# Performance work log

Hardware: AMD Instinct MI355X
Metric: run time of the kernel (lower is better)

## Reference

```python
import jax, jax.numpy as jnp
import numpy as np

N_NODES = 50000
LEAK = 0.01  # torch F.leaky_relu default negative_slope


def _gcn_conv(xg, ei, W, b):
    # Standard GCNConv: add self-loops, symmetric deg^-1/2 normalization, scatter-add.
    # xg: [N, 10], ei: [2, E] int
    n = xg.shape[0]
    loop = jnp.arange(n, dtype=ei.dtype)
    src = jnp.concatenate([ei[0], loop])  # [E+N]
    dst = jnp.concatenate([ei[1], loop])
    deg = jax.ops.segment_sum(jnp.ones_like(dst, dtype=xg.dtype), dst, num_segments=n)
    dinv = jnp.where(deg > 0, jax.lax.rsqrt(jnp.maximum(deg, 1.0)), 0.0)
    h = xg @ W  # [N, 10]
    norm = (dinv[src] * dinv[dst])[:, None]  # [E+N, 1]
    out = jax.ops.segment_sum(h[src] * norm, dst, num_segments=n)  # [N, 10]
    return out + b


def setup_inputs() -> dict:
    key = jax.random.key(0)
    ks = jax.random.split(key, 12)
    B, N, E = 32, N_NODES, 800000
    in_dim, out_dim = 20, 4
    x = jax.random.normal(ks[0], (B, in_dim // 2), dtype=jnp.float32)
    gcn_x = jax.random.normal(ks[1], (B, N, 10), dtype=jnp.float32)
    gcn_edge_index = jax.random.randint(ks[2], (B, 2, E), 0, N, dtype=jnp.int64 if jax.config.jax_enable_x64 else jnp.int32)
    s = lambda fan_in: 1.0 / np.sqrt(fan_in)
    W_gcn = jax.random.uniform(ks[3], (10, 10), jnp.float32, -s(10), s(10))
    b_gcn = jax.random.uniform(ks[4], (10,), jnp.float32, -s(10), s(10))
    W1 = jax.random.uniform(ks[5], (in_dim, 4 * in_dim), jnp.float32, -s(in_dim), s(in_dim))
    b1 = jax.random.uniform(ks[6], (4 * in_dim,), jnp.float32, -s(in_dim), s(in_dim))
    W2 = jax.random.uniform(ks[7], (4 * in_dim, 8 * in_dim), jnp.float32, -s(4 * in_dim), s(4 * in_dim))
    b2 = jax.random.uniform(ks[8], (8 * in_dim,), jnp.float32, -s(4 * in_dim), s(4 * in_dim))
    Wo = jax.random.uniform(ks[9], (8 * in_dim, out_dim), jnp.float32, -s(8 * in_dim), s(8 * in_dim))
    bo = jax.random.uniform(ks[10], (out_dim,), jnp.float32, -s(8 * in_dim), s(8 * in_dim))
    return {"x": x, "gcn_x": gcn_x, "gcn_edge_index": gcn_edge_index,
            "W_gcn": W_gcn, "b_gcn": b_gcn, "W1": W1, "b1": b1,
            "W2": W2, "b2": b2, "Wo": Wo, "bo": bo}


def reference(x, gcn_x, gcn_edge_index, W_gcn, b_gcn, W1, b1, W2, b2, Wo, bo):
    # batched GCN over independent graphs (vectorized version of the per-sample loop)
    gcn_out = jax.vmap(lambda xg, ei: _gcn_conv(xg, ei, W_gcn, b_gcn))(gcn_x, gcn_edge_index)
    pooled = jnp.mean(gcn_out, axis=1)  # [B, 10]
    h = jnp.concatenate([pooled, x], axis=1)  # [B, 20]
    h = jax.nn.leaky_relu(h @ W1 + b1, negative_slope=LEAK)
    h = jax.nn.leaky_relu(h @ W2 + b2, negative_slope=LEAK)
    h = jax.nn.log_softmax(h @ Wo + bo, axis=0)  # F.log_softmax(..., 0)
    return jnp.squeeze(h, axis=0) if h.shape[0] == 1 else h  # out_dim != 1 -> squeeze(0)
```

## Files before the change

kernel.cpp:

```cpp
#include <hip/hip_runtime.h>

#define N_NODES 50000
#define N_EDGES 800000
#define BATCH   32
#define NWORD8  12500
#define NWORDC  25000
#define CHUNKS  8
#define EPC4    25000
#define HCHUNKS 16
#define HEPC4   12500
#define QSCALE  255.0f
#define PTHREADS 640

__global__ __launch_bounds__(1024) void hist_kernel(const int* __restrict__ ei,
                                                    unsigned* __restrict__ partials) {
    const int chunk = blockIdx.x, b = blockIdx.y;
    __shared__ unsigned cnt[NWORD8];
    for (int i = threadIdx.x; i < NWORD8; i += 1024) cnt[i] = 0;
    __syncthreads();
    const int4* __restrict__ dst4 =
        (const int4*)(ei + (size_t)b * (2 * N_EDGES) + N_EDGES) + (size_t)chunk * HEPC4;
    for (int i = threadIdx.x; i < HEPC4; i += 1024) {
        const int4 v = dst4[i];
        atomicAdd(&cnt[((unsigned)v.x) >> 2], 1u << ((v.x & 3) * 8));
        atomicAdd(&cnt[((unsigned)v.y) >> 2], 1u << ((v.y & 3) * 8));
        atomicAdd(&cnt[((unsigned)v.z) >> 2], 1u << ((v.z & 3) * 8));
        atomicAdd(&cnt[((unsigned)v.w) >> 2], 1u << ((v.w & 3) * 8));
    }
    __syncthreads();
    unsigned* __restrict__ out = partials + (size_t)(b * HCHUNKS + chunk) * NWORD8;
    for (int i = threadIdx.x; i < NWORD8; i += 1024) out[i] = cnt[i];
}

__global__ void dinv_kernel(const unsigned* __restrict__ partials,
                            float* __restrict__ dinv,
                            unsigned* __restrict__ qd8) {
    const int idx = blockIdx.x * 256 + threadIdx.x;
    if (idx >= BATCH * NWORD8) return;
    const int b = idx / NWORD8, i = idx - b * NWORD8;
    const unsigned* __restrict__ p = partials + (size_t)(b * HCHUNKS) * NWORD8 + i;
    unsigned d0 = 0, d1 = 0, d2 = 0, d3 = 0;
#pragma unroll
    for (int c = 0; c < HCHUNKS; ++c) {
        const unsigned v = p[(size_t)c * NWORD8];
        d0 += v & 0xFF; d1 += (v >> 8) & 0xFF; d2 += (v >> 16) & 0xFF; d3 += v >> 24;
    }
    const float i0 = rsqrtf((float)(d0 + 1));
    const float i1 = rsqrtf((float)(d1 + 1));
    const float i2 = rsqrtf((float)(d2 + 1));
    const float i3 = rsqrtf((float)(d3 + 1));
    float4* dv4 = (float4*)(dinv + (size_t)b * N_NODES) + i;
    *dv4 = make_float4(i0, i1, i2, i3);
    const unsigned q0 = __float2uint_rn(i0 * QSCALE);
    const unsigned q1 = __float2uint_rn(i1 * QSCALE);
    const unsigned q2 = __float2uint_rn(i2 * QSCALE);
    const unsigned q3 = __float2uint_rn(i3 * QSCALE);
    qd8[(size_t)b * NWORD8 + i] = q0 | (q1 << 8) | (q2 << 16) | (q3 << 24);
}

__global__ __launch_bounds__(1024) void cscat_kernel(const int* __restrict__ ei,
                                                     const unsigned* __restrict__ qd8,
                                                     unsigned* __restrict__ cpart) {
    extern __shared__ unsigned smem[];
    unsigned* cs = smem;
    const unsigned char* qs = (const unsigned char*)(smem + NWORDC);
    const int id = blockIdx.x;
    const int b = (id & 7) + 8 * ((id >> 3) & 3);
    const int chunk = id >> 5;
    for (int i = threadIdx.x; i < NWORDC; i += 1024) cs[i] = 0;
    {
        const unsigned* __restrict__ src = qd8 + (size_t)b * NWORD8;
        unsigned* dst = smem + NWORDC;
        for (int i = threadIdx.x; i < NWORD8; i += 1024) dst[i] = src[i];
    }
    __syncthreads();
    const int* eb = ei + (size_t)b * (2 * N_EDGES);
    const int4* __restrict__ src4 = (const int4*)eb + (size_t)chunk * EPC4;
    const int4* __restrict__ dst4 = (const int4*)(eb + N_EDGES) + (size_t)chunk * EPC4;
    for (int i = threadIdx.x; i < EPC4; i += 1024) {
        const int4 s4 = src4[i];
        const int4 d4 = dst4[i];
        const unsigned q0 = qs[d4.x];
        const unsigned q1 = qs[d4.y];
        const unsigned q2 = qs[d4.z];
        const unsigned q3 = qs[d4.w];
        atomicAdd(&cs[((unsigned)s4.x) >> 1], q0 << ((s4.x & 1) << 4));
        atomicAdd(&cs[((unsigned)s4.y) >> 1], q1 << ((s4.y & 1) << 4));
        atomicAdd(&cs[((unsigned)s4.z) >> 1], q2 << ((s4.z & 1) << 4));
        atomicAdd(&cs[((unsigned)s4.w) >> 1], q3 << ((s4.w & 1) << 4));
    }
    __syncthreads();
    unsigned* __restrict__ out = cpart + (size_t)(b * CHUNKS + chunk) * NWORDC;
    for (int i = threadIdx.x; i < NWORDC; i += 1024) out[i] = cs[i];
}

__global__ void w_kernel(const unsigned* __restrict__ cpart,
                         const float* __restrict__ dinv,
                         float* __restrict__ w) {
    const int idx = blockIdx.x * 256 + threadIdx.x;
    if (idx >= BATCH * NWORDC) return;
    const int b = idx / NWORDC, i = idx - b * NWORDC;
    const unsigned* __restrict__ p = cpart + (size_t)(b * CHUNKS) * NWORDC + i;
    unsigned c0 = 0, c1 = 0;
#pragma unroll
    for (int c = 0; c < CHUNKS; ++c) {
        const unsigned v = p[(size_t)c * NWORDC];
        c0 += v & 0xFFFF; c1 += v >> 16;
    }
    const int node = 2 * i;
    const float2 d = *((const float2*)(dinv + (size_t)b * N_NODES + node));
    const float f0 = (float)c0 * (1.0f / QSCALE);
    const float f1 = (float)c1 * (1.0f / QSCALE);
    *((float2*)(w + (size_t)b * N_NODES + node)) = make_float2(d.x * (f0 + d.x), d.y * (f1 + d.y));
}

__global__ __launch_bounds__(PTHREADS) void pool_kernel(const float* __restrict__ xg,
                                                        const float* __restrict__ w,
                                                        float* __restrict__ spart) {
    const int chunk = blockIdx.x, b = blockIdx.y;
    const float4* __restrict__ xg4 = (const float4*)xg;
    const int base4 = b * 125000 + chunk * 15625;
    const int r = (4 * threadIdx.x) % 10;
    float a0 = 0.0f, a1 = 0.0f, a2 = 0.0f, a3 = 0.0f;
    for (int j = threadIdx.x; j < 15625; j += PTHREADS) {
        const int f4 = base4 + j;
        const int e0 = f4 * 4;
        const float4 v = xg4[f4];
        const float w0 = w[e0 / 10];
        const float w1 = (r == 8) ? w[e0 / 10 + 1] : w0;
        a0 += v.x * w0;
        a1 += v.y * w0;
        a2 += v.z * w1;
        a3 += v.w * w1;
    }
    __shared__ float sacc[PTHREADS / 64][10];
    const int wave = threadIdx.x >> 6;
    if ((threadIdx.x & 63) < 10) sacc[wave][threadIdx.x & 63] = 0.0f;
    __syncthreads();
    atomicAdd(&sacc[wave][r], a0);
    atomicAdd(&sacc[wave][(r + 1) % 10], a1);
    atomicAdd(&sacc[wave][(r + 2) % 10], a2);
    atomicAdd(&sacc[wave][(r + 3) % 10], a3);
    __syncthreads();
    if (threadIdx.x < 10) {
        float v = 0.0f;
#pragma unroll
        for (int wv = 0; wv < PTHREADS / 64; ++wv) v += sacc[wv][threadIdx.x];
        spart[(b * CHUNKS + chunk) * 16 + threadIdx.x] = v;
    }
}

__global__ __launch_bounds__(512) void mlp_kernel(const float* __restrict__ spart,
                           const float* __restrict__ x,
                           const float* __restrict__ W_gcn,
                           const float* __restrict__ b_gcn,
                           const float* __restrict__ W1, const float* __restrict__ b1,
                           const float* __restrict__ W2, const float* __restrict__ b2,
                           const float* __restrict__ Wo, const float* __restrict__ bo,
                           float* __restrict__ out) {
    __shared__ float ssum[32][10];
    __shared__ float h0[32][20];
    __shared__ float h1[32][80];
    __shared__ float h2[32][160];
    __shared__ float o[32][4];
    const int tid = threadIdx.x;

    for (int idx = tid; idx < 32 * 10; idx += blockDim.x) {
        const int b = idx / 10, k = idx % 10;
        float v = 0.0f;
#pragma unroll
        for (int c = 0; c < CHUNKS; ++c) v += spart[(b * CHUNKS + c) * 16 + k];
        ssum[b][k] = v;
    }
    __syncthreads();

    for (int idx = tid; idx < 32 * 20; idx += blockDim.x) {
        const int b = idx / 20, j = idx % 20;
        float v;
        if (j < 10) {
            v = 0.0f;
#pragma unroll
            for (int k = 0; k < 10; ++k) v += ssum[b][k] * W_gcn[k * 10 + j];
            v = v * (1.0f / (float)N_NODES) + b_gcn[j];
        } else {
            v = x[b * 10 + (j - 10)];
        }
        h0[b][j] = v;
    }
    __syncthreads();

    for (int idx = tid; idx < 32 * 80; idx += blockDim.x) {
        const int b = idx / 80, j = idx % 80;
        float v = b1[j];
#pragma unroll
        for (int k = 0; k < 20; ++k) v += h0[b][k] * W1[k * 80 + j];
        h1[b][j] = (v > 0.0f) ? v : 0.01f * v;
    }
    __syncthreads();

    for (int idx = tid; idx < 32 * 160; idx += blockDim.x) {
        const int b = idx / 160, j = idx % 160;
        float v = b2[j];
        for (int k = 0; k < 80; ++k) v += h1[b][k] * W2[k * 160 + j];
        h2[b][j] = (v > 0.0f) ? v : 0.01f * v;
    }
    __syncthreads();

    for (int idx = tid; idx < 32 * 4; idx += blockDim.x) {
        const int b = idx / 4, j = idx % 4;
        float v = bo[j];
        for (int k = 0; k < 160; ++k) v += h2[b][k] * Wo[k * 4 + j];
        o[b][j] = v;
    }
    __syncthreads();

    if (tid < 4) {
        float m = -1e30f;
        for (int b = 0; b < 32; ++b) m = fmaxf(m, o[b][tid]);
        float lse = 0.0f;
        for (int b = 0; b < 32; ++b) lse += expf(o[b][tid] - m);
        lse = logf(lse);
        for (int b = 0; b < 32; ++b) out[b * 4 + tid] = o[b][tid] - m - lse;
    }
}

extern "C" void kernel_launch(void* const* d_in, const int* in_sizes, int n_in,
                              void* d_out, int out_size, void* d_ws, size_t ws_size,
                              hipStream_t stream) {
    const float* x      = (const float*)d_in[0];
    const float* gcn_x  = (const float*)d_in[1];
    const int*   ei     = (const int*)d_in[2];
    const float* W_gcn  = (const float*)d_in[3];
    const float* b_gcn  = (const float*)d_in[4];
    const float* W1     = (const float*)d_in[5];
    const float* b1     = (const float*)d_in[6];
    const float* W2     = (const float*)d_in[7];
    const float* b2     = (const float*)d_in[8];
    const float* Wo     = (const float*)d_in[9];
    const float* bo     = (const float*)d_in[10];
    float* out = (float*)d_out;

    unsigned* partials = (unsigned*)d_ws;
    float*    dinv     = (float*)((char*)d_ws + (size_t)512 * NWORD8 * 4);
    unsigned* qd8      = (unsigned*)((char*)dinv + (size_t)BATCH * N_NODES * 4);
    float*    w        = (float*)((char*)qd8 + (size_t)BATCH * NWORD8 * 4);
    float*    spart    = (float*)((char*)w + (size_t)BATCH * N_NODES * 4);

    hipFuncSetAttribute((const void*)cscat_kernel,
                        hipFuncAttributeMaxDynamicSharedMemorySize,
                        (NWORDC + NWORD8) * 4);

    {
        dim3 grid(HCHUNKS, BATCH);
        hist_kernel<<<grid, 1024, 0, stream>>>(ei, partials);
    }
    {
        const int n = BATCH * NWORD8;
        dinv_kernel<<<(n + 255) / 256, 256, 0, stream>>>(partials, dinv, qd8);
    }
    {
        cscat_kernel<<<256, 1024, (NWORDC + NWORD8) * 4, stream>>>(ei, qd8, partials);
    }
    {
        const int n = BATCH * NWORDC;
        w_kernel<<<(n + 255) / 256, 256, 0, stream>>>(partials, dinv, w);
    }
    {
        dim3 grid(CHUNKS, BATCH);
        pool_kernel<<<grid, PTHREADS, 0, stream>>>(gcn_x, w, spart);
    }
    mlp_kernel<<<1, 512, 0, stream>>>(spart, x, W_gcn, b_gcn, W1, b1, W2, b2, Wo, bo, out);
}
```

Baseline: 409.3 us.

## Fuse all GCN stages into one cooperative persistent kernel with grid syncs

Replaces six separate launches with a single cooperative kernel of 256 blocks that runs the histogram, normalization, scatter, pooling and MLP phases, separated by grid.sync. The per-node weights are now computed into LDS inside the pooling phase rather than written to global memory and read back, and the histogram is split into 8 chunks instead of 16. This removes launch gaps and a global round trip for w, at the cost of grid-wide barriers, a single block running the MLP tail, and a requirement that all 256 blocks be co-resident.

```diff
diff --git a/kernel.cpp b/kernel.cpp
--- a/kernel.cpp
+++ b/kernel.cpp
@@ -1,4 +1,7 @@
 #include <hip/hip_runtime.h>
+#include <hip/hip_cooperative_groups.h>
+
+namespace cg = cooperative_groups;
 
 #define N_NODES 50000
 #define N_EDGES 800000
@@ -7,226 +10,228 @@
 #define NWORDC  25000
 #define CHUNKS  8
 #define EPC4    25000
-#define HCHUNKS 16
-#define HEPC4   12500
 #define QSCALE  255.0f
-#define PTHREADS 640
-
-__global__ __launch_bounds__(1024) void hist_kernel(const int* __restrict__ ei,
-                                                    unsigned* __restrict__ partials) {
-    const int chunk = blockIdx.x, b = blockIdx.y;
-    __shared__ unsigned cnt[NWORD8];
-    for (int i = threadIdx.x; i < NWORD8; i += 1024) cnt[i] = 0;
-    __syncthreads();
-    const int4* __restrict__ dst4 =
-        (const int4*)(ei + (size_t)b * (2 * N_EDGES) + N_EDGES) + (size_t)chunk * HEPC4;
-    for (int i = threadIdx.x; i < HEPC4; i += 1024) {
-        const int4 v = dst4[i];
-        atomicAdd(&cnt[((unsigned)v.x) >> 2], 1u << ((v.x & 3) * 8));
-        atomicAdd(&cnt[((unsigned)v.y) >> 2], 1u << ((v.y & 3) * 8));
-        atomicAdd(&cnt[((unsigned)v.z) >> 2], 1u << ((v.z & 3) * 8));
-        atomicAdd(&cnt[((unsigned)v.w) >> 2], 1u << ((v.w & 3) * 8));
-    }
-    __syncthreads();
-    unsigned* __restrict__ out = partials + (size_t)(b * HCHUNKS + chunk) * NWORD8;
-    for (int i = threadIdx.x; i < NWORD8; i += 1024) out[i] = cnt[i];
-}
-
-__global__ void dinv_kernel(const unsigned* __restrict__ partials,
-                            float* __restrict__ dinv,
-                            unsigned* __restrict__ qd8) {
-    const int idx = blockIdx.x * 256 + threadIdx.x;
-    if (idx >= BATCH * NWORD8) return;
-    const int b = idx / NWORD8, i = idx - b * NWORD8;
-    const unsigned* __restrict__ p = partials + (size_t)(b * HCHUNKS) * NWORD8 + i;
-    unsigned d0 = 0, d1 = 0, d2 = 0, d3 = 0;
-#pragma unroll
-    for (int c = 0; c < HCHUNKS; ++c) {
-        const unsigned v = p[(size_t)c * NWORD8];
-        d0 += v & 0xFF; d1 += (v >> 8) & 0xFF; d2 += (v >> 16) & 0xFF; d3 += v >> 24;
-    }
-    const float i0 = rsqrtf((float)(d0 + 1));
-    const float i1 = rsqrtf((float)(d1 + 1));
-    const float i2 = rsqrtf((float)(d2 + 1));
-    const float i3 = rsqrtf((float)(d3 + 1));
-    float4* dv4 = (float4*)(dinv + (size_t)b * N_NODES) + i;
-    *dv4 = make_float4(i0, i1, i2, i3);
-    const unsigned q0 = __float2uint_rn(i0 * QSCALE);
-    const unsigned q1 = __float2uint_rn(i1 * QSCALE);
-    const unsigned q2 = __float2uint_rn(i2 * QSCALE);
-    const unsigned q3 = __float2uint_rn(i3 * QSCALE);
-    qd8[(size_t)b * NWORD8 + i] = q0 | (q1 << 8) | (q2 << 16) | (q3 << 24);
-}
-
-__global__ __launch_bounds__(1024) void cscat_kernel(const int* __restrict__ ei,
-                                                     const unsigned* __restrict__ qd8,
-                                                     unsigned* __restrict__ cpart) {
+#define ACTIVE  1020
+#define DYNLDS  ((NWORDC + NWORD8) * 4)
+
+__global__ __launch_bounds__(1024, 1) void mega_kernel(
+    const int* __restrict__ ei, const float* __restrict__ xg,
+    const float* __restrict__ x,
+    const float* __restrict__ W_gcn, const float* __restrict__ b_gcn,
+    const float* __restrict__ W1, const float* __restrict__ b1,
+    const float* __restrict__ W2, const float* __restrict__ b2,
+    const float* __restrict__ Wo, const float* __restrict__ bo,
+    unsigned* __restrict__ partials,
+    float* __restrict__ dinv,
+    unsigned* __restrict__ qd8,
+    float* __restrict__ spart,
+    float* __restrict__ out)
+{
     extern __shared__ unsigned smem[];
-    unsigned* cs = smem;
-    const unsigned char* qs = (const unsigned char*)(smem + NWORDC);
-    const int id = blockIdx.x;
-    const int b = (id & 7) + 8 * ((id >> 3) & 3);
-    const int chunk = id >> 5;
-    for (int i = threadIdx.x; i < NWORDC; i += 1024) cs[i] = 0;
+    cg::grid_group grid = cg::this_grid();
+    const int bid = blockIdx.x;
+    const int tid = threadIdx.x;
+
     {
-        const unsigned* __restrict__ src = qd8 + (size_t)b * NWORD8;
-        unsigned* dst = smem + NWORDC;
-        for (int i = threadIdx.x; i < NWORD8; i += 1024) dst[i] = src[i];
-    }
-    __syncthreads();
-    const int* eb = ei + (size_t)b * (2 * N_EDGES);
-    const int4* __restrict__ src4 = (const int4*)eb + (size_t)chunk * EPC4;
-    const int4* __restrict__ dst4 = (const int4*)(eb + N_EDGES) + (size_t)chunk * EPC4;
-    for (int i = threadIdx.x; i < EPC4; i += 1024) {
-        const int4 s4 = src4[i];
-        const int4 d4 = dst4[i];
-        const unsigned q0 = qs[d4.x];
-        const unsigned q1 = qs[d4.y];
-        const unsigned q2 = qs[d4.z];
-        const unsigned q3 = qs[d4.w];
-        atomicAdd(&cs[((unsigned)s4.x) >> 1], q0 << ((s4.x & 1) << 4));
-        atomicAdd(&cs[((unsigned)s4.y) >> 1], q1 << ((s4.y & 1) << 4));
-        atomicAdd(&cs[((unsigned)s4.z) >> 1], q2 << ((s4.z & 1) << 4));
-        atomicAdd(&cs[((unsigned)s4.w) >> 1], q3 << ((s4.w & 1) << 4));
-    }
-    __syncthreads();
-    unsigned* __restrict__ out = cpart + (size_t)(b * CHUNKS + chunk) * NWORDC;
-    for (int i = threadIdx.x; i < NWORDC; i += 1024) out[i] = cs[i];
-}
-
-__global__ void w_kernel(const unsigned* __restrict__ cpart,
-                         const float* __restrict__ dinv,
-                         float* __restrict__ w) {
-    const int idx = blockIdx.x * 256 + threadIdx.x;
-    if (idx >= BATCH * NWORDC) return;
-    const int b = idx / NWORDC, i = idx - b * NWORDC;
-    const unsigned* __restrict__ p = cpart + (size_t)(b * CHUNKS) * NWORDC + i;
-    unsigned c0 = 0, c1 = 0;
-#pragma unroll
-    for (int c = 0; c < CHUNKS; ++c) {
-        const unsigned v = p[(size_t)c * NWORDC];
-        c0 += v & 0xFFFF; c1 += v >> 16;
-    }
-    const int node = 2 * i;
-    const float2 d = *((const float2*)(dinv + (size_t)b * N_NODES + node));
-    const float f0 = (float)c0 * (1.0f / QSCALE);
-    const float f1 = (float)c1 * (1.0f / QSCALE);
-    *((float2*)(w + (size_t)b * N_NODES + node)) = make_float2(d.x * (f0 + d.x), d.y * (f1 + d.y));
-}
-
-__global__ __launch_bounds__(PTHREADS) void pool_kernel(const float* __restrict__ xg,
-                                                        const float* __restrict__ w,
-                                                        float* __restrict__ spart) {
-    const int chunk = blockIdx.x, b = blockIdx.y;
-    const float4* __restrict__ xg4 = (const float4*)xg;
-    const int base4 = b * 125000 + chunk * 15625;
-    const int r = (4 * threadIdx.x) % 10;
-    float a0 = 0.0f, a1 = 0.0f, a2 = 0.0f, a3 = 0.0f;
-    for (int j = threadIdx.x; j < 15625; j += PTHREADS) {
-        const int f4 = base4 + j;
-        const int e0 = f4 * 4;
-        const float4 v = xg4[f4];
-        const float w0 = w[e0 / 10];
-        const float w1 = (r == 8) ? w[e0 / 10 + 1] : w0;
-        a0 += v.x * w0;
-        a1 += v.y * w0;
-        a2 += v.z * w1;
-        a3 += v.w * w1;
-    }
-    __shared__ float sacc[PTHREADS / 64][10];
-    const int wave = threadIdx.x >> 6;
-    if ((threadIdx.x & 63) < 10) sacc[wave][threadIdx.x & 63] = 0.0f;
-    __syncthreads();
-    atomicAdd(&sacc[wave][r], a0);
-    atomicAdd(&sacc[wave][(r + 1) % 10], a1);
-    atomicAdd(&sacc[wave][(r + 2) % 10], a2);
-    atomicAdd(&sacc[wave][(r + 3) % 10], a3);
-    __syncthreads();
-    if (threadIdx.x < 10) {
-        float v = 0.0f;
-#pragma unroll
-        for (int wv = 0; wv < PTHREADS / 64; ++wv) v += sacc[wv][threadIdx.x];
-        spart[(b * CHUNKS + chunk) * 16 + threadIdx.x] = v;
-    }
-}
-
-__global__ __launch_bounds__(512) void mlp_kernel(const float* __restrict__ spart,
-                           const float* __restrict__ x,
-                           const float* __restrict__ W_gcn,
-                           const float* __restrict__ b_gcn,
-                           const float* __restrict__ W1, const float* __restrict__ b1,
-                           const float* __restrict__ W2, const float* __restrict__ b2,
-                           const float* __restrict__ Wo, const float* __restrict__ bo,
-                           float* __restrict__ out) {
-    __shared__ float ssum[32][10];
-    __shared__ float h0[32][20];
-    __shared__ float h1[32][80];
-    __shared__ float h2[32][160];
-    __shared__ float o[32][4];
-    const int tid = threadIdx.x;
-
-    for (int idx = tid; idx < 32 * 10; idx += blockDim.x) {
-        const int b = idx / 10, k = idx % 10;
-        float v = 0.0f;
-#pragma unroll
-        for (int c = 0; c < CHUNKS; ++c) v += spart[(b * CHUNKS + c) * 16 + k];
-        ssum[b][k] = v;
-    }
-    __syncthreads();
-
-    for (int idx = tid; idx < 32 * 20; idx += blockDim.x) {
-        const int b = idx / 20, j = idx % 20;
-        float v;
-        if (j < 10) {
-            v = 0.0f;
-#pragma unroll
-            for (int k = 0; k < 10; ++k) v += ssum[b][k] * W_gcn[k * 10 + j];
-            v = v * (1.0f / (float)N_NODES) + b_gcn[j];
-        } else {
-            v = x[b * 10 + (j - 10)];
-        }
-        h0[b][j] = v;
-    }
-    __syncthreads();
-
-    for (int idx = tid; idx < 32 * 80; idx += blockDim.x) {
-        const int b = idx / 80, j = idx % 80;
-        float v = b1[j];
-#pragma unroll
-        for (int k = 0; k < 20; ++k) v += h0[b][k] * W1[k * 80 + j];
-        h1[b][j] = (v > 0.0f) ? v : 0.01f * v;
-    }
-    __syncthreads();
-
-    for (int idx = tid; idx < 32 * 160; idx += blockDim.x) {
-        const int b = idx / 160, j = idx % 160;
-        float v = b2[j];
-        for (int k = 0; k < 80; ++k) v += h1[b][k] * W2[k * 160 + j];
-        h2[b][j] = (v > 0.0f) ? v : 0.01f * v;
-    }
-    __syncthreads();
-
-    for (int idx = tid; idx < 32 * 4; idx += blockDim.x) {
-        const int b = idx / 4, j = idx % 4;
-        float v = bo[j];
-        for (int k = 0; k < 160; ++k) v += h2[b][k] * Wo[k * 4 + j];
-        o[b][j] = v;
-    }
-    __syncthreads();
-
-    if (tid < 4) {
-        float m = -1e30f;
-        for (int b = 0; b < 32; ++b) m = fmaxf(m, o[b][tid]);
-        float lse = 0.0f;
-        for (int b = 0; b < 32; ++b) lse += expf(o[b][tid] - m);
-        lse = logf(lse);
-        for (int b = 0; b < 32; ++b) out[b * 4 + tid] = o[b][tid] - m - lse;
+        unsigned* cnt = smem;
+        for (int i = tid; i < NWORD8; i += 1024) cnt[i] = 0;
+        __syncthreads();
+        const int b = bid >> 3, oct = bid & 7;
+        const int4* __restrict__ dst4 =
+            (const int4*)(ei + (size_t)b * (2 * N_EDGES) + N_EDGES) + (size_t)oct * EPC4;
+        for (int i = tid; i < EPC4; i += 1024) {
+            const int4 v = dst4[i];
+            atomicAdd(&cnt[((unsigned)v.x) >> 2], 1u << ((v.x & 3) * 8));
+            atomicAdd(&cnt[((unsigned)v.y) >> 2], 1u << ((v.y & 3) * 8));
+            atomicAdd(&cnt[((unsigned)v.z) >> 2], 1u << ((v.z & 3) * 8));
+            atomicAdd(&cnt[((unsigned)v.w) >> 2], 1u << ((v.w & 3) * 8));
+        }
+        __syncthreads();
+        unsigned* __restrict__ o8 = partials + (size_t)bid * NWORD8;
+        for (int i = tid; i < NWORD8; i += 1024) o8[i] = cnt[i];
+    }
+    __threadfence();
+    grid.sync();
+
+    for (int idx = bid * 1024 + tid; idx < BATCH * NWORD8; idx += 256 * 1024) {
+        const int b = idx / NWORD8, i = idx - b * NWORD8;
+        const unsigned* __restrict__ p = partials + (size_t)(b * CHUNKS) * NWORD8 + i;
+        unsigned d0 = 0, d1 = 0, d2 = 0, d3 = 0;
+#pragma unroll
+        for (int c = 0; c < CHUNKS; ++c) {
+            const unsigned v = p[(size_t)c * NWORD8];
+            d0 += v & 0xFF; d1 += (v >> 8) & 0xFF; d2 += (v >> 16) & 0xFF; d3 += v >> 24;
+        }
+        const float i0 = rsqrtf((float)(d0 + 1));
+        const float i1 = rsqrtf((float)(d1 + 1));
+        const float i2 = rsqrtf((float)(d2 + 1));
+        const float i3 = rsqrtf((float)(d3 + 1));
+        float4* dv4 = (float4*)(dinv + (size_t)b * N_NODES) + i;
+        *dv4 = make_float4(i0, i1, i2, i3);
+        const unsigned q0 = __float2uint_rn(i0 * QSCALE);
+        const unsigned q1 = __float2uint_rn(i1 * QSCALE);
+        const unsigned q2 = __float2uint_rn(i2 * QSCALE);
+        const unsigned q3 = __float2uint_rn(i3 * QSCALE);
+        qd8[(size_t)b * NWORD8 + i] = q0 | (q1 << 8) | (q2 << 16) | (q3 << 24);
+    }
+    __threadfence();
+    grid.sync();
+
+    {
+        unsigned* cs = smem;
+        const unsigned char* qs = (const unsigned char*)(smem + NWORDC);
+        const int b = bid & 31, chunk = bid >> 5;
+        for (int i = tid; i < NWORDC; i += 1024) cs[i] = 0;
+        const unsigned* __restrict__ qsrc = qd8 + (size_t)b * NWORD8;
+        for (int i = tid; i < NWORD8; i += 1024) smem[NWORDC + i] = qsrc[i];
+        __syncthreads();
+        const int* eb = ei + (size_t)b * (2 * N_EDGES);
+        const int4* __restrict__ s4p = (const int4*)eb + (size_t)chunk * EPC4;
+        const int4* __restrict__ d4p = (const int4*)(eb + N_EDGES) + (size_t)chunk * EPC4;
+        for (int i = tid; i < EPC4; i += 1024) {
+            const int4 s4 = s4p[i];
+            const int4 d4 = d4p[i];
+            const unsigned q0 = qs[d4.x];
+            const unsigned q1 = qs[d4.y];
+            const unsigned q2 = qs[d4.z];
+            const unsigned q3 = qs[d4.w];
+            atomicAdd(&cs[((unsigned)s4.x) >> 1], q0 << ((s4.x & 1) << 4));
+            atomicAdd(&cs[((unsigned)s4.y) >> 1], q1 << ((s4.y & 1) << 4));
+            atomicAdd(&cs[((unsigned)s4.z) >> 1], q2 << ((s4.z & 1) << 4));
+            atomicAdd(&cs[((unsigned)s4.w) >> 1], q3 << ((s4.w & 1) << 4));
+        }
+        __syncthreads();
+        unsigned* __restrict__ op = partials + (size_t)(b * CHUNKS + chunk) * NWORDC;
+        for (int i = tid; i < NWORDC; i += 1024) op[i] = cs[i];
+    }
+    __threadfence();
+    grid.sync();
+
+    {
+        float* wlds = (float*)smem;
+        float* sacc = (float*)smem + 6256;
+        const int c = bid & 7, b = bid >> 3;
+        const int wbase = c * (NWORDC / 8);
+        for (int i = tid; i < NWORDC / 8; i += 1024) {
+            const unsigned* __restrict__ p =
+                partials + (size_t)(b * CHUNKS) * NWORDC + wbase + i;
+            unsigned c0 = 0, c1 = 0;
+#pragma unroll
+            for (int ch = 0; ch < CHUNKS; ++ch) {
+                const unsigned v = p[(size_t)ch * NWORDC];
+                c0 += v & 0xFFFF; c1 += v >> 16;
+            }
+            const int node = 2 * (wbase + i);
+            const float2 d = *((const float2*)(dinv + (size_t)b * N_NODES + node));
+            wlds[2 * i]     = d.x * ((float)c0 * (1.0f / QSCALE) + d.x);
+            wlds[2 * i + 1] = d.y * ((float)c1 * (1.0f / QSCALE) + d.y);
+        }
+        const int wave = tid >> 6;
+        if ((tid & 63) < 10) sacc[wave * 10 + (tid & 63)] = 0.0f;
+        __syncthreads();
+        if (tid < ACTIVE) {
+            const float4* __restrict__ xg4 = (const float4*)xg;
+            const int base4 = b * 125000 + c * 15625;
+            const int r = (4 * tid) % 10;
+            float a0 = 0.0f, a1 = 0.0f, a2 = 0.0f, a3 = 0.0f;
+            for (int j = tid; j < 15625; j += ACTIVE) {
+                const float4 v = xg4[base4 + j];
+                const int ln = (4 * j) / 10;
+                const float w0 = wlds[ln];
+                const float w1 = (r == 8) ? wlds[ln + 1] : w0;
+                a0 += v.x * w0;
+                a1 += v.y * w0;
+                a2 += v.z * w1;
+                a3 += v.w * w1;
+            }
+            atomicAdd(&sacc[wave * 10 + r], a0);
+            atomicAdd(&sacc[wave * 10 + (r + 1) % 10], a1);
+            atomicAdd(&sacc[wave * 10 + (r + 2) % 10], a2);
+            atomicAdd(&sacc[wave * 10 + (r + 3) % 10], a3);
+        }
+        __syncthreads();
+        if (tid < 10) {
+            float v = 0.0f;
+#pragma unroll
+            for (int wv = 0; wv < 16; ++wv) v += sacc[wv * 10 + tid];
+            spart[(b * CHUNKS + c) * 16 + tid] = v;
+        }
+    }
+    __threadfence();
+    grid.sync();
+
+    if (bid == 0) {
+        float* fs   = (float*)smem;
+        float* ssum = fs;
+        float* h0   = fs + 320;
+        float* h1   = fs + 960;
+        float* h2   = fs + 3520;
+        float* o    = fs + 8640;
+
+        for (int idx = tid; idx < 32 * 10; idx += 1024) {
+            const int b = idx / 10, k = idx % 10;
+            float v = 0.0f;
+#pragma unroll
+            for (int c = 0; c < CHUNKS; ++c) v += spart[(b * CHUNKS + c) * 16 + k];
+            ssum[b * 10 + k] = v;
+        }
+        __syncthreads();
+
+        for (int idx = tid; idx < 32 * 20; idx += 1024) {
+            const int b = idx / 20, j = idx % 20;
+            float v;
+            if (j < 10) {
+                v = 0.0f;
+#pragma unroll
+                for (int k = 0; k < 10; ++k) v += ssum[b * 10 + k] * W_gcn[k * 10 + j];
+                v = v * (1.0f / (float)N_NODES) + b_gcn[j];
+            } else {
+                v = x[b * 10 + (j - 10)];
+            }
+            h0[b * 20 + j] = v;
+        }
+        __syncthreads();
+
+        for (int idx = tid; idx < 32 * 80; idx += 1024) {
+            const int b = idx / 80, j = idx % 80;
+            float v = b1[j];
+#pragma unroll
+            for (int k = 0; k < 20; ++k) v += h0[b * 20 + k] * W1[k * 80 + j];
+            h1[b * 80 + j] = (v > 0.0f) ? v : 0.01f * v;
+        }
+        __syncthreads();
+
+        for (int idx = tid; idx < 32 * 160; idx += 1024) {
+            const int b = idx / 160, j = idx % 160;
+            float v = b2[j];
+            for (int k = 0; k < 80; ++k) v += h1[b * 80 + k] * W2[k * 160 + j];
+            h2[b * 160 + j] = (v > 0.0f) ? v : 0.01f * v;
+        }
+        __syncthreads();
+
+        for (int idx = tid; idx < 32 * 4; idx += 1024) {
+            const int b = idx / 4, j = idx % 4;
+            float v = bo[j];
+            for (int k = 0; k < 160; ++k) v += h2[b * 160 + k] * Wo[k * 4 + j];
+            o[b * 4 + j] = v;
+        }
+        __syncthreads();
+
+        if (tid < 4) {
+            float m = -1e30f;
+            for (int b = 0; b < 32; ++b) m = fmaxf(m, o[b * 4 + tid]);
+            float lse = 0.0f;
+            for (int b = 0; b < 32; ++b) lse += expf(o[b * 4 + tid] - m);
+            lse = logf(lse);
+            for (int b = 0; b < 32; ++b) out[b * 4 + tid] = o[b * 4 + tid] - m - lse;
+        }
     }
 }
 
 extern "C" void kernel_launch(void* const* d_in, const int* in_sizes, int n_in,
                               void* d_out, int out_size, void* d_ws, size_t ws_size,
                               hipStream_t stream) {
+    (void)in_sizes; (void)n_in; (void)out_size; (void)ws_size;
     const float* x      = (const float*)d_in[0];
     const float* gcn_x  = (const float*)d_in[1];
     const int*   ei     = (const int*)d_in[2];
@@ -241,33 +246,20 @@
     float* out = (float*)d_out;
 
     unsigned* partials = (unsigned*)d_ws;
-    float*    dinv     = (float*)((char*)d_ws + (size_t)512 * NWORD8 * 4);
+    float*    dinv     = (float*)((char*)d_ws + (size_t)BATCH * CHUNKS * NWORDC * 4);
     unsigned* qd8      = (unsigned*)((char*)dinv + (size_t)BATCH * N_NODES * 4);
-    float*    w        = (float*)((char*)qd8 + (size_t)BATCH * NWORD8 * 4);
-    float*    spart    = (float*)((char*)w + (size_t)BATCH * N_NODES * 4);
-
-    hipFuncSetAttribute((const void*)cscat_kernel,
-                        hipFuncAttributeMaxDynamicSharedMemorySize,
-                        (NWORDC + NWORD8) * 4);
-
-    {
-        dim3 grid(HCHUNKS, BATCH);
-        hist_kernel<<<grid, 1024, 0, stream>>>(ei, partials);
-    }
-    {
-        const int n = BATCH * NWORD8;
-        dinv_kernel<<<(n + 255) / 256, 256, 0, stream>>>(partials, dinv, qd8);
-    }
-    {
-        cscat_kernel<<<256, 1024, (NWORDC + NWORD8) * 4, stream>>>(ei, qd8, partials);
-    }
-    {
-        const int n = BATCH * NWORDC;
-        w_kernel<<<(n + 255) / 256, 256, 0, stream>>>(partials, dinv, w);
-    }
-    {
-        dim3 grid(CHUNKS, BATCH);
-        pool_kernel<<<grid, PTHREADS, 0, stream>>>(gcn_x, w, spart);
-    }
-    mlp_kernel<<<1, 512, 0, stream>>>(spart, x, W_gcn, b_gcn, W1, b1, W2, b2, Wo, bo, out);
+    float*    spart    = (float*)((char*)qd8 + (size_t)BATCH * NWORD8 * 4);
+
+    hipFuncSetAttribute((const void*)mega_kernel,
+                        hipFuncAttributeMaxDynamicSharedMemorySize, DYNLDS);
+
+    void* args[] = {
+        (void*)&ei, (void*)&gcn_x, (void*)&x,
+        (void*)&W_gcn, (void*)&b_gcn,
+        (void*)&W1, (void*)&b1, (void*)&W2, (void*)&b2,
+        (void*)&Wo, (void*)&bo,
+        (void*)&partials, (void*)&dinv, (void*)&qd8, (void*)&spart, (void*)&out
+    };
+    hipLaunchCooperativeKernel((void*)mega_kernel, dim3(256), dim3(1024),
+                               args, DYNLDS, stream);
 }
```

Result: slower. 899.1 us (+119.7%).

## Fuse weight, pooling and MLP kernels with last-block completion counter

Applied to the files above, without the earlier changes.

The per-node weight computation is folded into the pooling kernel: each block builds its slice of weights in LDS instead of a separate kernel writing and re-reading a global weight array. The MLP tail now runs in whichever block finishes last, detected through an atomic counter that the dinv kernel resets, which removes two kernel launches. The pooling block grows to 1024 threads with 1020 active. The shared-memory attribute call is also cached in a static flag. The cost is a serialized single-block MLP tail plus threadfence and atomic overhead.

```diff
diff --git a/kernel.cpp b/kernel.cpp
--- a/kernel.cpp
+++ b/kernel.cpp
@@ -10,7 +10,7 @@
 #define HCHUNKS 16
 #define HEPC4   12500
 #define QSCALE  255.0f
-#define PTHREADS 640
+#define ACTIVE  1020
 
 __global__ __launch_bounds__(1024) void hist_kernel(const int* __restrict__ ei,
                                                     unsigned* __restrict__ partials) {
@@ -34,8 +34,10 @@
 
 __global__ void dinv_kernel(const unsigned* __restrict__ partials,
                             float* __restrict__ dinv,
-                            unsigned* __restrict__ qd8) {
+                            unsigned* __restrict__ qd8,
+                            unsigned* __restrict__ done) {
     const int idx = blockIdx.x * 256 + threadIdx.x;
+    if (idx == 0) *done = 0u;
     if (idx >= BATCH * NWORD8) return;
     const int b = idx / NWORD8, i = idx - b * NWORD8;
     const unsigned* __restrict__ p = partials + (size_t)(b * HCHUNKS) * NWORD8 + i;
@@ -94,139 +96,146 @@
     for (int i = threadIdx.x; i < NWORDC; i += 1024) out[i] = cs[i];
 }
 
-__global__ void w_kernel(const unsigned* __restrict__ cpart,
-                         const float* __restrict__ dinv,
-                         float* __restrict__ w) {
-    const int idx = blockIdx.x * 256 + threadIdx.x;
-    if (idx >= BATCH * NWORDC) return;
-    const int b = idx / NWORDC, i = idx - b * NWORDC;
-    const unsigned* __restrict__ p = cpart + (size_t)(b * CHUNKS) * NWORDC + i;
-    unsigned c0 = 0, c1 = 0;
-#pragma unroll
-    for (int c = 0; c < CHUNKS; ++c) {
-        const unsigned v = p[(size_t)c * NWORDC];
-        c0 += v & 0xFFFF; c1 += v >> 16;
-    }
-    const int node = 2 * i;
-    const float2 d = *((const float2*)(dinv + (size_t)b * N_NODES + node));
-    const float f0 = (float)c0 * (1.0f / QSCALE);
-    const float f1 = (float)c1 * (1.0f / QSCALE);
-    *((float2*)(w + (size_t)b * N_NODES + node)) = make_float2(d.x * (f0 + d.x), d.y * (f1 + d.y));
-}
-
-__global__ __launch_bounds__(PTHREADS) void pool_kernel(const float* __restrict__ xg,
-                                                        const float* __restrict__ w,
-                                                        float* __restrict__ spart) {
-    const int chunk = blockIdx.x, b = blockIdx.y;
-    const float4* __restrict__ xg4 = (const float4*)xg;
-    const int base4 = b * 125000 + chunk * 15625;
-    const int r = (4 * threadIdx.x) % 10;
-    float a0 = 0.0f, a1 = 0.0f, a2 = 0.0f, a3 = 0.0f;
-    for (int j = threadIdx.x; j < 15625; j += PTHREADS) {
-        const int f4 = base4 + j;
-        const int e0 = f4 * 4;
-        const float4 v = xg4[f4];
-        const float w0 = w[e0 / 10];
-        const float w1 = (r == 8) ? w[e0 / 10 + 1] : w0;
-        a0 += v.x * w0;
-        a1 += v.y * w0;
-        a2 += v.z * w1;
-        a3 += v.w * w1;
-    }
-    __shared__ float sacc[PTHREADS / 64][10];
-    const int wave = threadIdx.x >> 6;
-    if ((threadIdx.x & 63) < 10) sacc[wave][threadIdx.x & 63] = 0.0f;
-    __syncthreads();
-    atomicAdd(&sacc[wave][r], a0);
-    atomicAdd(&sacc[wave][(r + 1) % 10], a1);
-    atomicAdd(&sacc[wave][(r + 2) % 10], a2);
-    atomicAdd(&sacc[wave][(r + 3) % 10], a3);
-    __syncthreads();
-    if (threadIdx.x < 10) {
+__global__ __launch_bounds__(1024) void poolw_kernel(
+    const unsigned* __restrict__ cpart, const float* __restrict__ dinv,
+    const float* __restrict__ xg, const float* __restrict__ x,
+    const float* __restrict__ W_gcn, const float* __restrict__ b_gcn,
+    const float* __restrict__ W1, const float* __restrict__ b1,
+    const float* __restrict__ W2, const float* __restrict__ b2,
+    const float* __restrict__ Wo, const float* __restrict__ bo,
+    float* __restrict__ spart, unsigned* __restrict__ done,
+    float* __restrict__ out)
+{
+    __shared__ float smf[8768];
+    __shared__ unsigned lastf;
+    const int c = blockIdx.x, b = blockIdx.y;
+    const int tid = threadIdx.x;
+    float* wlds = smf;
+    float* sacc = smf + 6256;
+
+    const int wbase = c * (NWORDC / 8);
+    for (int i = tid; i < NWORDC / 8; i += 1024) {
+        const unsigned* __restrict__ p =
+            cpart + (size_t)(b * CHUNKS) * NWORDC + wbase + i;
+        unsigned c0 = 0, c1 = 0;
+#pragma unroll
+        for (int ch = 0; ch < CHUNKS; ++ch) {
+            const unsigned v = p[(size_t)ch * NWORDC];
+            c0 += v & 0xFFFF; c1 += v >> 16;
+        }
+        const int node = 2 * (wbase + i);
+        const float2 d = *((const float2*)(dinv + (size_t)b * N_NODES + node));
+        wlds[2 * i]     = d.x * ((float)c0 * (1.0f / QSCALE) + d.x);
+        wlds[2 * i + 1] = d.y * ((float)c1 * (1.0f / QSCALE) + d.y);
+    }
+    const int wave = tid >> 6;
+    if ((tid & 63) < 10) sacc[wave * 10 + (tid & 63)] = 0.0f;
+    __syncthreads();
+
+    if (tid < ACTIVE) {
+        const float4* __restrict__ xg4 = (const float4*)xg;
+        const int base4 = b * 125000 + c * 15625;
+        const int r = (4 * tid) % 10;
+        float a0 = 0.0f, a1 = 0.0f, a2 = 0.0f, a3 = 0.0f;
+        for (int j = tid; j < 15625; j += ACTIVE) {
+            const float4 v = xg4[base4 + j];
+            const int ln = (4 * j) / 10;
+            const float w0 = wlds[ln];
+            const float w1 = (r == 8) ? wlds[ln + 1] : w0;
+            a0 += v.x * w0;
+            a1 += v.y * w0;
+            a2 += v.z * w1;
+            a3 += v.w * w1;
+        }
+        atomicAdd(&sacc[wave * 10 + r], a0);
+        atomicAdd(&sacc[wave * 10 + (r + 1) % 10], a1);
+        atomicAdd(&sacc[wave * 10 + (r + 2) % 10], a2);
+        atomicAdd(&sacc[wave * 10 + (r + 3) % 10], a3);
+    }
+    __syncthreads();
+    if (tid < 10) {
         float v = 0.0f;
 #pragma unroll
-        for (int wv = 0; wv < PTHREADS / 64; ++wv) v += sacc[wv][threadIdx.x];
-        spart[(b * CHUNKS + chunk) * 16 + threadIdx.x] = v;
-    }
-}
-
-__global__ __launch_bounds__(512) void mlp_kernel(const float* __restrict__ spart,
-                           const float* __restrict__ x,
-                           const float* __restrict__ W_gcn,
-                           const float* __restrict__ b_gcn,
-                           const float* __restrict__ W1, const float* __restrict__ b1,
-                           const float* __restrict__ W2, const float* __restrict__ b2,
-                           const float* __restrict__ Wo, const float* __restrict__ bo,
-                           float* __restrict__ out) {
-    __shared__ float ssum[32][10];
-    __shared__ float h0[32][20];
-    __shared__ float h1[32][80];
-    __shared__ float h2[32][160];
-    __shared__ float o[32][4];
-    const int tid = threadIdx.x;
-
-    for (int idx = tid; idx < 32 * 10; idx += blockDim.x) {
-        const int b = idx / 10, k = idx % 10;
+        for (int wv = 0; wv < 16; ++wv) v += sacc[wv * 10 + tid];
+        spart[(b * CHUNKS + c) * 16 + tid] = v;
+    }
+
+    __threadfence();
+    __syncthreads();
+    if (tid == 0) lastf = (atomicAdd(done, 1u) == (unsigned)(8 * BATCH - 1));
+    __syncthreads();
+    if (!lastf) return;
+    __threadfence();
+
+    float* ssum = smf;
+    float* h0   = smf + 320;
+    float* h1   = smf + 960;
+    float* h2   = smf + 3520;
+    float* o    = smf + 8640;
+
+    for (int idx = tid; idx < 32 * 10; idx += 1024) {
+        const int bb = idx / 10, k = idx % 10;
         float v = 0.0f;
 #pragma unroll
-        for (int c = 0; c < CHUNKS; ++c) v += spart[(b * CHUNKS + c) * 16 + k];
-        ssum[b][k] = v;
-    }
-    __syncthreads();
-
-    for (int idx = tid; idx < 32 * 20; idx += blockDim.x) {
-        const int b = idx / 20, j = idx % 20;
+        for (int ch = 0; ch < CHUNKS; ++ch) v += spart[(bb * CHUNKS + ch) * 16 + k];
+        ssum[bb * 10 + k] = v;
+    }
+    __syncthreads();
+
+    for (int idx = tid; idx < 32 * 20; idx += 1024) {
+        const int bb = idx / 20, j = idx % 20;
         float v;
         if (j < 10) {
             v = 0.0f;
 #pragma unroll
-            for (int k = 0; k < 10; ++k) v += ssum[b][k] * W_gcn[k * 10 + j];
+            for (int k = 0; k < 10; ++k) v += ssum[bb * 10 + k] * W_gcn[k * 10 + j];
             v = v * (1.0f / (float)N_NODES) + b_gcn[j];
         } else {
-            v = x[b * 10 + (j - 10)];
+            v = x[bb * 10 + (j - 10)];
         }
-        h0[b][j] = v;
-    }
-    __syncthreads();
-
-    for (int idx = tid; idx < 32 * 80; idx += blockDim.x) {
-        const int b = idx / 80, j = idx % 80;
+        h0[bb * 20 + j] = v;
+    }
+    __syncthreads();
+
+    for (int idx = tid; idx < 32 * 80; idx += 1024) {
+        const int bb = idx / 80, j = idx % 80;
         float v = b1[j];
 #pragma unroll
-        for (int k = 0; k < 20; ++k) v += h0[b][k] * W1[k * 80 + j];
-        h1[b][j] = (v > 0.0f) ? v : 0.01f * v;
-    }
-    __syncthreads();
-
-    for (int idx = tid; idx < 32 * 160; idx += blockDim.x) {
-        const int b = idx / 160, j = idx % 160;
+        for (int k = 0; k < 20; ++k) v += h0[bb * 20 + k] * W1[k * 80 + j];
+        h1[bb * 80 + j] = (v > 0.0f) ? v : 0.01f * v;
+    }
+    __syncthreads();
+
+    for (int idx = tid; idx < 32 * 160; idx += 1024) {
+        const int bb = idx / 160, j = idx % 160;
         float v = b2[j];
-        for (int k = 0; k < 80; ++k) v += h1[b][k] * W2[k * 160 + j];
-        h2[b][j] = (v > 0.0f) ? v : 0.01f * v;
-    }
-    __syncthreads();
-
-    for (int idx = tid; idx < 32 * 4; idx += blockDim.x) {
-        const int b = idx / 4, j = idx % 4;
+        for (int k = 0; k < 80; ++k) v += h1[bb * 80 + k] * W2[k * 160 + j];
+        h2[bb * 160 + j] = (v > 0.0f) ? v : 0.01f * v;
+    }
+    __syncthreads();
+
+    for (int idx = tid; idx < 32 * 4; idx += 1024) {
+        const int bb = idx / 4, j = idx % 4;
         float v = bo[j];
-        for (int k = 0; k < 160; ++k) v += h2[b][k] * Wo[k * 4 + j];
-        o[b][j] = v;
+        for (int k = 0; k < 160; ++k) v += h2[bb * 160 + k] * Wo[k * 4 + j];
+        o[bb * 4 + j] = v;
     }
     __syncthreads();
 
     if (tid < 4) {
         float m = -1e30f;
-        for (int b = 0; b < 32; ++b) m = fmaxf(m, o[b][tid]);
+        for (int bb = 0; bb < 32; ++bb) m = fmaxf(m, o[bb * 4 + tid]);
         float lse = 0.0f;
-        for (int b = 0; b < 32; ++b) lse += expf(o[b][tid] - m);
+        for (int bb = 0; bb < 32; ++bb) lse += expf(o[bb * 4 + tid] - m);
         lse = logf(lse);
-        for (int b = 0; b < 32; ++b) out[b * 4 + tid] = o[b][tid] - m - lse;
+        for (int bb = 0; bb < 32; ++bb) out[bb * 4 + tid] = o[bb * 4 + tid] - m - lse;
     }
 }
 
 extern "C" void kernel_launch(void* const* d_in, const int* in_sizes, int n_in,
                               void* d_out, int out_size, void* d_ws, size_t ws_size,
                               hipStream_t stream) {
+    (void)in_sizes; (void)n_in; (void)out_size; (void)ws_size;
     const float* x      = (const float*)d_in[0];
     const float* gcn_x  = (const float*)d_in[1];
     const int*   ei     = (const int*)d_in[2];
@@ -243,12 +252,16 @@
     unsigned* partials = (unsigned*)d_ws;
     float*    dinv     = (float*)((char*)d_ws + (size_t)512 * NWORD8 * 4);
     unsigned* qd8      = (unsigned*)((char*)dinv + (size_t)BATCH * N_NODES * 4);
-    float*    w        = (float*)((char*)qd8 + (size_t)BATCH * NWORD8 * 4);
-    float*    spart    = (float*)((char*)w + (size_t)BATCH * N_NODES * 4);
-
-    hipFuncSetAttribute((const void*)cscat_kernel,
-                        hipFuncAttributeMaxDynamicSharedMemorySize,
-                        (NWORDC + NWORD8) * 4);
+    float*    spart    = (float*)((char*)qd8 + (size_t)BATCH * NWORD8 * 4);
+    unsigned* done     = (unsigned*)((char*)spart + (size_t)BATCH * CHUNKS * 16 * 4);
+
+    static bool attr_set = false;
+    if (!attr_set) {
+        hipFuncSetAttribute((const void*)cscat_kernel,
+                            hipFuncAttributeMaxDynamicSharedMemorySize,
+                            (NWORDC + NWORD8) * 4);
+        attr_set = true;
+    }
 
     {
         dim3 grid(HCHUNKS, BATCH);
@@ -256,18 +269,15 @@
     }
     {
         const int n = BATCH * NWORD8;
-        dinv_kernel<<<(n + 255) / 256, 256, 0, stream>>>(partials, dinv, qd8);
+        dinv_kernel<<<(n + 255) / 256, 256, 0, stream>>>(partials, dinv, qd8, done);
     }
     {
         cscat_kernel<<<256, 1024, (NWORDC + NWORD8) * 4, stream>>>(ei, qd8, partials);
     }
     {
-        const int n = BATCH * NWORDC;
-        w_kernel<<<(n + 255) / 256, 256, 0, stream>>>(partials, dinv, w);
-    }
-    {
         dim3 grid(CHUNKS, BATCH);
-        pool_kernel<<<grid, PTHREADS, 0, stream>>>(gcn_x, w, spart);
-    }
-    mlp_kernel<<<1, 512, 0, stream>>>(spart, x, W_gcn, b_gcn, W1, b1, W2, b2, Wo, bo, out);
-}
+        poolw_kernel<<<grid, 1024, 0, stream>>>(partials, dinv, gcn_x, x,
+                                                W_gcn, b_gcn, W1, b1, W2, b2, Wo, bo,
+                                                spart, done, out);
+    }
+}
```

New measurement: 457.6 us. 1.12x slower.
